# Kernel tuning notes

Measured on AMD Instinct MI355X. Metric: run time of the kernel, lower is better.

The kernel has to match this reference:

```python
import jax, jax.numpy as jnp
import numpy as np

N_NODES = 100000
N_EDGES = 3200000
NDIM_IN = 64
EDIM = 64
NDIM_OUT = 32
HID1, HID2 = 50, 25


def _linear_init(key, fan_in, fan_out):
    # torch nn.Linear default: U(-1/sqrt(fan_in), 1/sqrt(fan_in))
    kw, kb = jax.random.split(key)
    bound = 1.0 / np.sqrt(fan_in)
    W = jax.random.uniform(kw, (fan_in, fan_out), jnp.float32, -bound, bound)
    b = jax.random.uniform(kb, (fan_out,), jnp.float32, -bound, bound)
    return W, b


def setup_inputs() -> dict:
    key = jax.random.key(0)
    ks = jax.random.split(key, 10)
    nfeats = jax.random.normal(ks[0], (N_NODES, 1, NDIM_IN), jnp.float32)
    efeats = jax.random.normal(ks[1], (N_EDGES, 1, EDIM), jnp.float32)
    src = jax.random.randint(ks[2], (N_EDGES,), 0, N_NODES, jnp.int32)
    dst = jax.random.randint(ks[3], (N_EDGES,), 0, N_NODES, jnp.int32)
    Wm1, bm1 = _linear_init(ks[4], NDIM_IN + EDIM, HID1)
    Wa1, ba1 = _linear_init(ks[5], NDIM_IN + HID1, HID1)
    Wm2, bm2 = _linear_init(ks[6], HID1 + EDIM, HID2)
    Wa2, ba2 = _linear_init(ks[7], HID1 + HID2, HID2)
    Wm3, bm3 = _linear_init(ks[8], HID2 + EDIM, NDIM_OUT)
    Wa3, ba3 = _linear_init(ks[9], HID2 + NDIM_OUT, NDIM_OUT)
    return {
        "nfeats": nfeats, "efeats": efeats, "src": src, "dst": dst,
        "Wm1": Wm1, "bm1": bm1, "Wa1": Wa1, "ba1": ba1,
        "Wm2": Wm2, "bm2": bm2, "Wa2": Wa2, "ba2": ba2,
        "Wm3": Wm3, "bm3": bm3, "Wa3": Wa3, "ba3": ba3,
    }


def _gnn_layer(h, e, src, dst, Wm, bm, Wa, ba):
    # h: [N,1,Fin], e: [E,1,Fe]
    # per-edge message: relu(Linear(cat(h[src], e)))  -> [E,1,Fout]
    m = jax.nn.relu(jnp.concatenate([h[src], e], axis=-1) @ Wm + bm)
    # sum-aggregate messages per destination node -> [N,1,Fout]
    h_neigh = jax.ops.segment_sum(m, dst, num_segments=h.shape[0])
    # node apply: relu(Linear(cat(h, h_neigh)))
    return jax.nn.relu(jnp.concatenate([h, h_neigh], axis=-1) @ Wa + ba)


def reference(nfeats, efeats, src, dst,
              Wm1, bm1, Wa1, ba1,
              Wm2, bm2, Wa2, ba2,
              Wm3, bm3, Wa3, ba3):
    h = _gnn_layer(nfeats, efeats, src, dst, Wm1, bm1, Wa1, ba1)
    h = _gnn_layer(h, efeats, src, dst, Wm2, bm2, Wa2, ba2)  # dropout p=0.0
    h = _gnn_layer(h, efeats, src, dst, Wm3, bm3, Wa3, ba3)
    return h.sum(axis=1)  # [N, ndim_out]
```

## Files before the change

### kernel.cpp

```cpp
#include <hip/hip_runtime.h>

#define DEVINL __device__ __forceinline__

typedef __attribute__((ext_vector_type(8))) short bf16x8;
typedef __attribute__((ext_vector_type(4))) float f32x4;

DEVINL void fma4(float4& a, const float4 w, const float x) {
    a.x += w.x * x; a.y += w.y * x; a.z += w.z * x; a.w += w.w * x;
}

DEVINL unsigned short bf16of(float x) {
    unsigned a = __float_as_uint(x);
    a += 0x7FFFu + ((a >> 16) & 1u);
    return (unsigned short)(a >> 16);
}

DEVINL unsigned bfpair(float lo, float hi) {
    unsigned a = __float_as_uint(lo);
    a += 0x7FFFu + ((a >> 16) & 1u);
    unsigned b = __float_as_uint(hi);
    b += 0x7FFFu + ((b >> 16) & 1u);
    return (a >> 16) | (b & 0xFFFF0000u);
}

DEVINL float bflo(unsigned u) { return __uint_as_float(u << 16); }
DEVINL float bfhi(unsigned u) { return __uint_as_float(u & 0xFFFF0000u); }

DEVINL bf16x8 as_bf16x8(uint4 u) {
    union { uint4 u4; bf16x8 b; } cv; cv.u4 = u; return cv.b;
}

__global__ __launch_bounds__(256) void hist_kernel(const int* __restrict__ d,
                                                   int* __restrict__ counts, int n) {
    for (int i = blockIdx.x * 256 + threadIdx.x; i < n; i += gridDim.x * 256)
        atomicAdd(&counts[d[i]], 1);
}

__global__ __launch_bounds__(1024) void scan_block(const int* __restrict__ in,
                                                   int* __restrict__ out,
                                                   int* __restrict__ bsums, int n) {
    __shared__ int buf[2][1024];
    const int t = threadIdx.x;
    const int i = blockIdx.x * 1024 + t;
    const int v = (i < n) ? in[i] : 0;
    int cur = 0;
    buf[0][t] = v;
    __syncthreads();
    #pragma unroll
    for (int s = 1; s < 1024; s <<= 1) {
        int x = buf[cur][t];
        if (t >= s) x += buf[cur][t - s];
        buf[cur ^ 1][t] = x;
        cur ^= 1;
        __syncthreads();
    }
    if (i < n) out[i] = buf[cur][t] - v;
    if (t == 1023) bsums[blockIdx.x] = buf[cur][t];
}

__global__ void scan_small(int* __restrict__ bs, int nb) {
    if (blockIdx.x == 0 && threadIdx.x == 0) {
        int acc = 0;
        for (int i = 0; i < nb; i++) { int v = bs[i]; bs[i] = acc; acc += v; }
    }
}

__global__ __launch_bounds__(1024) void add_offsets(int* __restrict__ out,
                                                    const int* __restrict__ bs, int n) {
    int i = blockIdx.x * 1024 + threadIdx.x;
    if (i < n) out[i] += bs[blockIdx.x];
}

__global__ __launch_bounds__(256) void scatter_kernel(const int* __restrict__ d,
                                                      const int* __restrict__ src,
                                                      int* __restrict__ cursor,
                                                      int4* __restrict__ recs, int n) {
    for (int i = blockIdx.x * 256 + threadIdx.x; i < n; i += gridDim.x * 256) {
        int dd = d[i];
        int ss = src[i];
        int pos = atomicAdd(&cursor[dd], 1);
        recs[pos] = make_int4(i, dd, ss, 0);
    }
}

template<int FIN, int FOUT, int FOUTP>
__global__ __launch_bounds__(256) void pack_we(const float* __restrict__ W,
                                               float* __restrict__ Wp) {
    int idx = blockIdx.x * 256 + threadIdx.x;
    if (idx >= 64 * FOUTP) return;
    int k = idx / FOUTP, j = idx - k * FOUTP;
    Wp[idx] = (j < FOUT) ? W[(FIN + k) * FOUT + j] : 0.f;
}

template<int FIN, int FOUT, int NC>
__global__ __launch_bounds__(256) void pack_wbt(const float* __restrict__ W,
                                                unsigned short* __restrict__ WbT) {
    int idx = blockIdx.x * 256 + threadIdx.x;
    if (idx >= NC * 64) return;
    int c = idx / 64, k = idx - c * 64;
    WbT[idx] = (c < FOUT) ? bf16of(W[(FIN + k) * FOUT + c]) : (unsigned short)0;
}

template<int FIN, int FOUT, int FOUTP>
__global__ __launch_bounds__(256) void gemv_g(
    const float* __restrict__ x,
    const float* __restrict__ W,
    const float* __restrict__ b,
    float* __restrict__ g, int nNodes)
{
    constexpr int F4 = FOUTP / 4;
    __shared__ float4 Wl[FIN * F4];
    __shared__ float  bl[FOUTP];
    const int tid = threadIdx.x;
    for (int idx = tid; idx < FIN * FOUTP; idx += 256) {
        int k = idx / FOUTP, j = idx - k * FOUTP;
        reinterpret_cast<float*>(Wl)[idx] = (j < FOUT) ? W[k * FOUT + j] : 0.f;
    }
    for (int idx = tid; idx < FOUTP; idx += 256)
        bl[idx] = (idx < FOUT) ? b[idx] : 0.f;
    __syncthreads();
    const int n = blockIdx.x * 256 + tid;
    if (n >= nNodes) return;
    float4 acc[F4];
    #pragma unroll
    for (int j4 = 0; j4 < F4; j4++) acc[j4] = reinterpret_cast<float4*>(bl)[j4];
    const float* xr = x + (long long)n * FIN;
    #pragma unroll 1
    for (int k = 0; k < FIN; ++k) {
        float xk = xr[k];
        const float4* wrow = &Wl[k * F4];
        #pragma unroll
        for (int j4 = 0; j4 < F4; j4++) fma4(acc[j4], wrow[j4], xk);
    }
    float4* gr = reinterpret_cast<float4*>(g + (long long)n * FOUTP);
    #pragma unroll
    for (int j4 = 0; j4 < F4; j4++) gr[j4] = acc[j4];
}

__global__ __launch_bounds__(256) void edge_mfma_all(
    const float* __restrict__ g,
    const float* __restrict__ efeats,
    const int4* __restrict__ recs,
    const unsigned short* __restrict__ Wb1,
    const unsigned short* __restrict__ Wb2,
    const unsigned short* __restrict__ Wb3,
    unsigned* __restrict__ ep2,
    unsigned* __restrict__ ep3,
    float* __restrict__ agg)
{
    constexpr int FOUT = 50, FOUTP = 52, NT = 4;
    constexpr int MS = NT * 16 + 1;

    __shared__ float msg[4][32 * MS];
    __shared__ int eidL[512], sIdxL[512], dseg[512];

    const int tid = threadIdx.x;
    const long long pb = (long long)blockIdx.x * 512;
    {
        int4 r0 = recs[pb + tid];
        int4 r1 = recs[pb + 256 + tid];
        eidL[tid] = r0.x;  dseg[tid] = r0.y;  sIdxL[tid] = r0.z;
        eidL[tid + 256] = r1.x; dseg[tid + 256] = r1.y; sIdxL[tid + 256] = r1.z;
    }
    __syncthreads();

    const int lane = tid & 63;
    const int wv   = tid >> 6;
    const int lg   = lane >> 4;
    const int lc   = lane & 15;

    bf16x8 bfr1[2][4], bfr2[2][2], bfr3[2][2];
    #pragma unroll
    for (int kt = 0; kt < 2; kt++) {
        #pragma unroll
        for (int nt = 0; nt < 4; nt++)
            bfr1[kt][nt] = *reinterpret_cast<const bf16x8*>(Wb1 + (nt * 16 + lc) * 64 + kt * 32 + lg * 8);
        #pragma unroll
        for (int nt = 0; nt < 2; nt++) {
            bfr2[kt][nt] = *reinterpret_cast<const bf16x8*>(Wb2 + (nt * 16 + lc) * 64 + kt * 32 + lg * 8);
            bfr3[kt][nt] = *reinterpret_cast<const bf16x8*>(Wb3 + (nt * 16 + lc) * 64 + kt * 32 + lg * 8);
        }
    }

    float* msgW = msg[wv];

    #pragma unroll 1
    for (int ch = 0; ch < 4; ++ch) {
        const int rb0 = wv * 128 + ch * 32;
        #pragma unroll 1
        for (int mt = 0; mt < 2; ++mt) {
            const int rowbase = rb0 + mt * 16;
            const long long tix = (pb >> 4) + wv * 8 + ch * 2 + mt;
            const int eid = eidL[rowbase + lc];
            const float4* erow = reinterpret_cast<const float4*>(efeats + (long long)eid * 64);
            float4 f0 = erow[lg * 2];
            float4 f1 = erow[lg * 2 + 1];
            float4 f2 = erow[8 + lg * 2];
            float4 f3 = erow[8 + lg * 2 + 1];
            uint4 u0, u1;
            u0.x = bfpair(f0.x, f0.y); u0.y = bfpair(f0.z, f0.w);
            u0.z = bfpair(f1.x, f1.y); u0.w = bfpair(f1.z, f1.w);
            u1.x = bfpair(f2.x, f2.y); u1.y = bfpair(f2.z, f2.w);
            u1.z = bfpair(f3.x, f3.y); u1.w = bfpair(f3.z, f3.w);
            bf16x8 a0 = as_bf16x8(u0);
            bf16x8 a1 = as_bf16x8(u1);

            int sr[4];
            #pragma unroll
            for (int r = 0; r < 4; r++) sr[r] = sIdxL[rowbase + lg * 4 + r];

            #pragma unroll
            for (int nt = 0; nt < 4; nt++) {
                f32x4 acc = {0.f, 0.f, 0.f, 0.f};
                acc = __builtin_amdgcn_mfma_f32_16x16x32_bf16(a0, bfr1[0][nt], acc, 0, 0, 0);
                acc = __builtin_amdgcn_mfma_f32_16x16x32_bf16(a1, bfr1[1][nt], acc, 0, 0, 0);
                const int col = nt * 16 + lc;
                #pragma unroll
                for (int r = 0; r < 4; r++) {
                    float gv = (col < FOUT) ? g[(long long)sr[r] * FOUTP + col] : 0.f;
                    msgW[(mt * 16 + lg * 4 + r) * MS + col] = fmaxf(acc[r] + gv, 0.f);
                }
            }
            {
                uint4 st;
                #pragma unroll
                for (int nt = 0; nt < 2; nt++) {
                    f32x4 acc = {0.f, 0.f, 0.f, 0.f};
                    acc = __builtin_amdgcn_mfma_f32_16x16x32_bf16(a0, bfr2[0][nt], acc, 0, 0, 0);
                    acc = __builtin_amdgcn_mfma_f32_16x16x32_bf16(a1, bfr2[1][nt], acc, 0, 0, 0);
                    unsigned w0 = bfpair(acc[0], acc[1]);
                    unsigned w1 = bfpair(acc[2], acc[3]);
                    if (nt == 0) { st.x = w0; st.y = w1; } else { st.z = w0; st.w = w1; }
                }
                reinterpret_cast<uint4*>(ep2)[tix * 64 + lane] = st;
            }
            {
                uint4 st;
                #pragma unroll
                for (int nt = 0; nt < 2; nt++) {
                    f32x4 acc = {0.f, 0.f, 0.f, 0.f};
                    acc = __builtin_amdgcn_mfma_f32_16x16x32_bf16(a0, bfr3[0][nt], acc, 0, 0, 0);
                    acc = __builtin_amdgcn_mfma_f32_16x16x32_bf16(a1, bfr3[1][nt], acc, 0, 0, 0);
                    unsigned w0 = bfpair(acc[0], acc[1]);
                    unsigned w1 = bfpair(acc[2], acc[3]);
                    if (nt == 0) { st.x = w0; st.y = w1; } else { st.z = w0; st.w = w1; }
                }
                reinterpret_cast<uint4*>(ep3)[tix * 64 + lane] = st;
            }
        }
        const int base = rb0;
        for (int r0 = 0; r0 < 32; ++r0) {
            int dr = dseg[base + r0];
            if (r0 > 0 && dseg[base + r0 - 1] == dr) continue;
            float s = 0.f;
            int rr = r0;
            while (true) {
                s += msgW[rr * MS + lane];
                ++rr;
                if (rr >= 32 || dseg[base + rr] != dr) break;
            }
            if (lane < FOUT) atomicAdd(agg + (long long)dr * FOUT + lane, s);
        }
    }
}

template<int FOUT, int FOUTP>
__global__ __launch_bounds__(256) void edge_ep(
    const float* __restrict__ g,
    const unsigned* __restrict__ ep,
    const int4* __restrict__ recs,
    float* __restrict__ agg)
{
    constexpr int NT = 2;
    constexpr int MS = NT * 16 + 1;

    __shared__ float msg[4][32 * MS];
    __shared__ int sIdxL[512], dseg[512];

    const int tid = threadIdx.x;
    const long long pb = (long long)blockIdx.x * 512;
    {
        int4 r0 = recs[pb + tid];
        int4 r1 = recs[pb + 256 + tid];
        dseg[tid] = r0.y;  sIdxL[tid] = r0.z;
        dseg[tid + 256] = r1.y; sIdxL[tid + 256] = r1.z;
    }
    __syncthreads();

    const int lane = tid & 63;
    const int wv   = tid >> 6;
    const int lg   = lane >> 4;
    const int lc   = lane & 15;

    float* msgW = msg[wv];

    #pragma unroll 1
    for (int ch = 0; ch < 4; ++ch) {
        const int rb0 = wv * 128 + ch * 32;
        #pragma unroll
        for (int mt = 0; mt < 2; ++mt) {
            const int rowbase = rb0 + mt * 16;
            const long long tix = (pb >> 4) + wv * 8 + ch * 2 + mt;
            uint4 v = reinterpret_cast<const uint4*>(ep)[tix * 64 + lane];

            int sr[4];
            #pragma unroll
            for (int r = 0; r < 4; r++) sr[r] = sIdxL[rowbase + lg * 4 + r];

            #pragma unroll
            for (int nt = 0; nt < 2; nt++) {
                float e0 = bflo(nt == 0 ? v.x : v.z);
                float e1 = bfhi(nt == 0 ? v.x : v.z);
                float e2 = bflo(nt == 0 ? v.y : v.w);
                float e3 = bfhi(nt == 0 ? v.y : v.w);
                const int col = nt * 16 + lc;
                float ev[4] = {e0, e1, e2, e3};
                #pragma unroll
                for (int r = 0; r < 4; r++) {
                    float gv = (col < FOUT) ? g[(long long)sr[r] * FOUTP + col] : 0.f;
                    msgW[(mt * 16 + lg * 4 + r) * MS + col] = fmaxf(ev[r] + gv, 0.f);
                }
            }
        }
        const int base = rb0;
        for (int r0 = 0; r0 < 32; ++r0) {
            int dr = dseg[base + r0];
            if (r0 > 0 && dseg[base + r0 - 1] == dr) continue;
            float s = 0.f;
            int rr = r0;
            while (true) {
                s += msgW[rr * MS + lane];
                ++rr;
                if (rr >= 32 || dseg[base + rr] != dr) break;
            }
            if (lane < FOUT) atomicAdd(agg + (long long)dr * FOUT + lane, s);
        }
    }
}

template<int FOUT, int FOUTP, int MS>
__global__ __launch_bounds__(256) void edge_fb(
    const float* __restrict__ g,
    const float* __restrict__ efeats,
    const int4* __restrict__ recs,
    const float* __restrict__ Wp,
    float* __restrict__ agg)
{
    constexpr int F4 = FOUTP / 4;
    constexpr int ST = 17;
    static_assert(128 * MS + 64 <= 512 * ST, "msg buf exceeds sbuf");

    __shared__ float sbuf[512 * ST];
    __shared__ int   dseg[512];

    const int tid = threadIdx.x;
    const long long pb = (long long)blockIdx.x * 512;
    int4 r0 = recs[pb + tid];
    int4 r1 = recs[pb + 256 + tid];
    dseg[tid] = r0.y;
    dseg[tid + 256] = r1.y;

    const float4* gr0 = reinterpret_cast<const float4*>(g + (long long)r0.z * FOUTP);
    const float4* gr1 = reinterpret_cast<const float4*>(g + (long long)r1.z * FOUTP);
    const float*  er0 = efeats + (long long)r0.x * 64;
    const float*  er1 = efeats + (long long)r1.x * 64;
    const float4* Wp4 = reinterpret_cast<const float4*>(Wp);

    float4 acc0[F4], acc1[F4];
    #pragma unroll
    for (int j4 = 0; j4 < F4; j4++) acc0[j4] = gr0[j4];
    #pragma unroll
    for (int j4 = 0; j4 < F4; j4++) acc1[j4] = gr1[j4];

    const int t0 = tid * ST;
    const int t1 = (tid + 256) * ST;

    for (int c = 0; c < 4; ++c) {
        const int off = c * 16;
        #pragma unroll
        for (int f = 0; f < 4; ++f) {
            float4 v0 = *reinterpret_cast<const float4*>(er0 + off + 4 * f);
            float4 v1 = *reinterpret_cast<const float4*>(er1 + off + 4 * f);
            float* d0 = &sbuf[t0 + 4 * f];
            float* d1 = &sbuf[t1 + 4 * f];
            d0[0] = v0.x; d0[1] = v0.y; d0[2] = v0.z; d0[3] = v0.w;
            d1[0] = v1.x; d1[1] = v1.y; d1[2] = v1.z; d1[3] = v1.w;
        }
        #pragma unroll 1
        for (int k = 0; k < 16; ++k) {
            const float x0 = sbuf[t0 + k];
            const float x1 = sbuf[t1 + k];
            const float4* wrow = &Wp4[(off + k) * F4];
            #pragma unroll
            for (int j4 = 0; j4 < F4; j4++) {
                float4 w = wrow[j4];
                fma4(acc0[j4], w, x0);
                fma4(acc1[j4], w, x1);
            }
        }
    }

    const int lane = tid & 63;
    const int wv   = tid >> 6;

    #pragma unroll 1
    for (int bb = 0; bb < 4; ++bb) {
        __syncthreads();
        if ((tid >> 7) == (bb & 1)) {
            const int r = tid & 127;
            float* mrow = &sbuf[r * MS];
            const float4* accp = (bb < 2) ? acc0 : acc1;
            #pragma unroll
            for (int j4 = 0; j4 < F4; j4++) {
                float4 a = accp[j4];
                if (4 * j4 + 0 < FOUT) mrow[4 * j4 + 0] = fmaxf(a.x, 0.f);
                if (4 * j4 + 1 < FOUT) mrow[4 * j4 + 1] = fmaxf(a.y, 0.f);
                if (4 * j4 + 2 < FOUT) mrow[4 * j4 + 2] = fmaxf(a.z, 0.f);
                if (4 * j4 + 3 < FOUT) mrow[4 * j4 + 3] = fmaxf(a.w, 0.f);
            }
        }
        __syncthreads();

        const int rbase = bb * 128;
        for (int r0i = wv * 32; r0i < wv * 32 + 32; ++r0i) {
            int dr = dseg[rbase + r0i];
            if (r0i > 0 && dseg[rbase + r0i - 1] == dr) continue;
            float s = 0.f;
            int rr = r0i;
            while (true) {
                s += sbuf[rr * MS + lane];
                ++rr;
                if (rr >= 128 || dseg[rbase + rr] != dr) break;
            }
            if (lane < FOUT) atomicAdd(agg + (long long)dr * FOUT + lane, s);
        }
    }
}

template<int FH, int FHP, int FAGG, int FOUT, int FOUTP, int GOUT, int GOUTP>
__global__ __launch_bounds__(256) void node_kernel(
    const float* __restrict__ h,
    const float* __restrict__ agg,
    const float* __restrict__ Wa,
    const float* __restrict__ ba,
    const float* __restrict__ Wmn,
    const float* __restrict__ bmn,
    float* __restrict__ out,
    float* __restrict__ gout,
    int nNodes)
{
    constexpr int K  = FH + FAGG;
    constexpr int F4 = FOUTP / 4;
    constexpr int G4 = (GOUT > 0) ? GOUTP / 4 : 1;

    __shared__ float4 Wl[K * F4];
    __shared__ float4 Wg[(GOUT > 0) ? FOUTP * G4 : 1];
    __shared__ float  bl[FOUTP];
    __shared__ float  bg[(GOUT > 0) ? GOUTP : 4];

    const int tid = threadIdx.x;
    for (int idx = tid; idx < K * FOUTP; idx += 256) {
        int k = idx / FOUTP, j = idx - k * FOUTP;
        reinterpret_cast<float*>(Wl)[idx] = (j < FOUT) ? Wa[k * FOUT + j] : 0.f;
    }
    for (int idx = tid; idx < FOUTP; idx += 256)
        bl[idx] = (idx < FOUT) ? ba[idx] : 0.f;
    if constexpr (GOUT > 0) {
        for (int idx = tid; idx < FOUTP * GOUTP; idx += 256) {
            int k = idx / GOUTP, j = idx - k * GOUTP;
            reinterpret_cast<float*>(Wg)[idx] =
                (k < FOUT && j < GOUT) ? Wmn[k * GOUT + j] : 0.f;
        }
        for (int idx = tid; idx < GOUTP; idx += 256)
            bg[idx] = (idx < GOUT) ? bmn[idx] : 0.f;
    }
    __syncthreads();

    const int n = blockIdx.x * 256 + tid;
    if (n >= nNodes) return;

    float4 acc[F4];
    #pragma unroll
    for (int j4 = 0; j4 < F4; j4++) acc[j4] = reinterpret_cast<float4*>(bl)[j4];

    const float* hrow = h + (long long)n * FHP;
    #pragma unroll 1
    for (int k = 0; k < FH; k++) {
        float xk = hrow[k];
        const float4* wrow = &Wl[k * F4];
        #pragma unroll
        for (int j4 = 0; j4 < F4; j4++) fma4(acc[j4], wrow[j4], xk);
    }
    const float* arow = agg + (long long)n * FAGG;
    #pragma unroll 1
    for (int k = 0; k < FAGG; k++) {
        float xk = arow[k];
        const float4* wrow = &Wl[(FH + k) * F4];
        #pragma unroll
        for (int j4 = 0; j4 < F4; j4++) fma4(acc[j4], wrow[j4], xk);
    }

    #pragma unroll
    for (int j4 = 0; j4 < F4; j4++) {
        acc[j4].x = fmaxf(acc[j4].x, 0.f);
        acc[j4].y = fmaxf(acc[j4].y, 0.f);
        acc[j4].z = fmaxf(acc[j4].z, 0.f);
        acc[j4].w = fmaxf(acc[j4].w, 0.f);
    }
    float4* orow = reinterpret_cast<float4*>(out + (long long)n * FOUTP);
    #pragma unroll
    for (int j4 = 0; j4 < F4; j4++) orow[j4] = acc[j4];

    if constexpr (GOUT > 0) {
        float4 gacc[G4];
        #pragma unroll
        for (int j4 = 0; j4 < G4; j4++) gacc[j4] = reinterpret_cast<float4*>(bg)[j4];
        #pragma unroll 1
        for (int k4 = 0; k4 < F4; ++k4) {
            float4 xv = acc[k4];
            #pragma unroll
            for (int c = 0; c < 4; ++c) {
                float xc = (c == 0) ? xv.x : (c == 1) ? xv.y : (c == 2) ? xv.z : xv.w;
                const float4* wrow = &Wg[(k4 * 4 + c) * G4];
                #pragma unroll
                for (int j4 = 0; j4 < G4; j4++) fma4(gacc[j4], wrow[j4], xc);
            }
        }
        float4* grow = reinterpret_cast<float4*>(gout + (long long)n * GOUTP);
        #pragma unroll
        for (int j4 = 0; j4 < G4; j4++) grow[j4] = gacc[j4];
    }
}

extern "C" void kernel_launch(void* const* d_in, const int* in_sizes, int n_in,
                              void* d_out, int out_size, void* d_ws, size_t ws_size,
                              hipStream_t stream)
{
    const float* nfeats = (const float*)d_in[0];
    const float* efeats = (const float*)d_in[1];
    const int*   src    = (const int*)d_in[2];
    const int*   dst    = (const int*)d_in[3];
    const float* Wm1 = (const float*)d_in[4],  *bm1 = (const float*)d_in[5];
    const float* Wa1 = (const float*)d_in[6],  *ba1 = (const float*)d_in[7];
    const float* Wm2 = (const float*)d_in[8],  *bm2 = (const float*)d_in[9];
    const float* Wa2 = (const float*)d_in[10], *ba2 = (const float*)d_in[11];
    const float* Wm3 = (const float*)d_in[12], *bm3 = (const float*)d_in[13];
    const float* Wa3 = (const float*)d_in[14], *ba3 = (const float*)d_in[15];
    float* out = (float*)d_out;

    constexpr int N = 100000;
    constexpr int E = 3200000;
    constexpr int SCAN_BLOCKS = (N + 1023) / 1024;

    float* ws   = (float*)d_ws;
    float* h1   = ws;
    float* h2   = h1 + (size_t)N * 52;
    float* agg  = h2 + (size_t)N * 28;
    float* g    = agg + (size_t)N * 52;
    int* counts = (int*)(g + (size_t)N * 52);
    int* cursor = counts + N;
    int* bsums  = cursor + N;
    int4* recs  = (int4*)(bsums + 128);
    float* Wp1  = (float*)(recs + E);
    float* Wp2  = Wp1 + 64 * 52;
    float* Wp3  = Wp2 + 64 * 28;
    unsigned short* Wb1 = (unsigned short*)(Wp3 + 64 * 32);
    unsigned short* Wb2 = Wb1 + 64 * 64;
    unsigned short* Wb3 = Wb2 + 32 * 64;
    char* endp = (char*)(Wb3 + 32 * 64);

    size_t usedB  = (size_t)(endp - (char*)d_ws);
    size_t epOffB = (usedB + 127) & ~(size_t)127;
    size_t neededB = epOffB + (size_t)E * 128;
    const bool useBf = (ws_size >= neededB);
    unsigned* ep2 = (unsigned*)((char*)d_ws + epOffB);
    unsigned* ep3 = ep2 + (size_t)E * 16;

    pack_we<64, 50, 52><<<(64 * 52 + 255) / 256, 256, 0, stream>>>(Wm1, Wp1);
    pack_we<50, 25, 28><<<(64 * 28 + 255) / 256, 256, 0, stream>>>(Wm2, Wp2);
    pack_we<25, 32, 32><<<(64 * 32 + 255) / 256, 256, 0, stream>>>(Wm3, Wp3);
    pack_wbt<64, 50, 64><<<(64 * 64 + 255) / 256, 256, 0, stream>>>(Wm1, Wb1);
    pack_wbt<50, 25, 32><<<(32 * 64 + 255) / 256, 256, 0, stream>>>(Wm2, Wb2);
    pack_wbt<25, 32, 32><<<(32 * 64 + 255) / 256, 256, 0, stream>>>(Wm3, Wb3);

    hipMemsetAsync(counts, 0, (size_t)N * sizeof(int), stream);
    hist_kernel<<<2048, 256, 0, stream>>>(dst, counts, E);
    scan_block<<<SCAN_BLOCKS, 1024, 0, stream>>>(counts, cursor, bsums, N);
    scan_small<<<1, 64, 0, stream>>>(bsums, SCAN_BLOCKS);
    add_offsets<<<SCAN_BLOCKS, 1024, 0, stream>>>(cursor, bsums, N);
    scatter_kernel<<<2048, 256, 0, stream>>>(dst, src, cursor, recs, E);

    const int EB = E / 512;
    const int NB = (N + 255) / 256;

    gemv_g<64, 50, 52><<<NB, 256, 0, stream>>>(nfeats, Wm1, bm1, g, N);

    hipMemsetAsync(agg, 0, (size_t)N * 52 * sizeof(float), stream);
    if (useBf)
        edge_mfma_all<<<EB, 256, 0, stream>>>(g, efeats, recs, Wb1, Wb2, Wb3, ep2, ep3, agg);
    else
        edge_fb<50, 52, 51><<<EB, 256, 0, stream>>>(g, efeats, recs, Wp1, agg);
    node_kernel<64, 64, 50, 50, 52, 25, 28><<<NB, 256, 0, stream>>>(
        nfeats, agg, Wa1, ba1, Wm2, bm2, h1, g, N);

    hipMemsetAsync(agg, 0, (size_t)N * 52 * sizeof(float), stream);
    if (useBf)
        edge_ep<25, 28><<<EB, 256, 0, stream>>>(g, ep2, recs, agg);
    else
        edge_fb<25, 28, 25><<<EB, 256, 0, stream>>>(g, efeats, recs, Wp2, agg);
    node_kernel<50, 52, 25, 25, 28, 32, 32><<<NB, 256, 0, stream>>>(
        h1, agg, Wa2, ba2, Wm3, bm3, h2, g, N);

    hipMemsetAsync(agg, 0, (size_t)N * 52 * sizeof(float), stream);
    if (useBf)
        edge_ep<32, 32><<<EB, 256, 0, stream>>>(g, ep3, recs, agg);
    else
        edge_fb<32, 32, 33><<<EB, 256, 0, stream>>>(g, efeats, recs, Wp3, agg);
    node_kernel<25, 28, 32, 32, 32, 0, 0><<<NB, 256, 0, stream>>>(
        h2, agg, Wa3, ba3, nullptr, nullptr, out, nullptr, N);
}
```

Baseline: 1.551 ms.

## Software-pipeline edge feature and gathered node loads across chunks in edge kernels

```diff
diff --git a/kernel.cpp b/kernel.cpp
--- a/kernel.cpp
+++ b/kernel.cpp
@@ -184,30 +184,49 @@
 
     float* msgW = msg[wv];
 
+    float4 f[2][4];
+    {
+        const int rb0 = wv * 128;
+        #pragma unroll
+        for (int mt = 0; mt < 2; mt++) {
+            const int eid = eidL[rb0 + mt * 16 + lc];
+            const float4* erow = reinterpret_cast<const float4*>(efeats + (long long)eid * 64);
+            f[mt][0] = erow[lg * 2];     f[mt][1] = erow[lg * 2 + 1];
+            f[mt][2] = erow[8 + lg * 2]; f[mt][3] = erow[8 + lg * 2 + 1];
+        }
+    }
+
     #pragma unroll 1
     for (int ch = 0; ch < 4; ++ch) {
         const int rb0 = wv * 128 + ch * 32;
-        #pragma unroll 1
-        for (int mt = 0; mt < 2; ++mt) {
-            const int rowbase = rb0 + mt * 16;
-            const long long tix = (pb >> 4) + wv * 8 + ch * 2 + mt;
-            const int eid = eidL[rowbase + lc];
-            const float4* erow = reinterpret_cast<const float4*>(efeats + (long long)eid * 64);
-            float4 f0 = erow[lg * 2];
-            float4 f1 = erow[lg * 2 + 1];
-            float4 f2 = erow[8 + lg * 2];
-            float4 f3 = erow[8 + lg * 2 + 1];
+
+        int srr[2][4];
+        #pragma unroll
+        for (int mt = 0; mt < 2; mt++)
+            #pragma unroll
+            for (int r = 0; r < 4; r++)
+                srr[mt][r] = sIdxL[rb0 + mt * 16 + lg * 4 + r];
+        float gv[2][NT][4];
+        #pragma unroll
+        for (int mt = 0; mt < 2; mt++)
+            #pragma unroll
+            for (int nt = 0; nt < NT; nt++) {
+                const int col = nt * 16 + lc;
+                #pragma unroll
+                for (int r = 0; r < 4; r++)
+                    gv[mt][nt][r] = (col < FOUT) ? g[(long long)srr[mt][r] * FOUTP + col] : 0.f;
+            }
+
+        #pragma unroll
+        for (int mt = 0; mt < 2; mt++) {
             uint4 u0, u1;
-            u0.x = bfpair(f0.x, f0.y); u0.y = bfpair(f0.z, f0.w);
-            u0.z = bfpair(f1.x, f1.y); u0.w = bfpair(f1.z, f1.w);
-            u1.x = bfpair(f2.x, f2.y); u1.y = bfpair(f2.z, f2.w);
-            u1.z = bfpair(f3.x, f3.y); u1.w = bfpair(f3.z, f3.w);
+            u0.x = bfpair(f[mt][0].x, f[mt][0].y); u0.y = bfpair(f[mt][0].z, f[mt][0].w);
+            u0.z = bfpair(f[mt][1].x, f[mt][1].y); u0.w = bfpair(f[mt][1].z, f[mt][1].w);
+            u1.x = bfpair(f[mt][2].x, f[mt][2].y); u1.y = bfpair(f[mt][2].z, f[mt][2].w);
+            u1.z = bfpair(f[mt][3].x, f[mt][3].y); u1.w = bfpair(f[mt][3].z, f[mt][3].w);
             bf16x8 a0 = as_bf16x8(u0);
             bf16x8 a1 = as_bf16x8(u1);
-
-            int sr[4];
-            #pragma unroll
-            for (int r = 0; r < 4; r++) sr[r] = sIdxL[rowbase + lg * 4 + r];
+            const long long tix = (pb >> 4) + wv * 8 + ch * 2 + mt;
 
             #pragma unroll
             for (int nt = 0; nt < 4; nt++) {
@@ -216,10 +235,8 @@
                 acc = __builtin_amdgcn_mfma_f32_16x16x32_bf16(a1, bfr1[1][nt], acc, 0, 0, 0);
                 const int col = nt * 16 + lc;
                 #pragma unroll
-                for (int r = 0; r < 4; r++) {
-                    float gv = (col < FOUT) ? g[(long long)sr[r] * FOUTP + col] : 0.f;
-                    msgW[(mt * 16 + lg * 4 + r) * MS + col] = fmaxf(acc[r] + gv, 0.f);
-                }
+                for (int r = 0; r < 4; r++)
+                    msgW[(mt * 16 + lg * 4 + r) * MS + col] = fmaxf(acc[r] + gv[mt][nt][r], 0.f);
             }
             {
                 uint4 st;
@@ -248,6 +265,19 @@
                 reinterpret_cast<uint4*>(ep3)[tix * 64 + lane] = st;
             }
         }
+
+        float4 fn[2][4];
+        if (ch < 3) {
+            const int rbn = wv * 128 + (ch + 1) * 32;
+            #pragma unroll
+            for (int mt = 0; mt < 2; mt++) {
+                const int eid = eidL[rbn + mt * 16 + lc];
+                const float4* erow = reinterpret_cast<const float4*>(efeats + (long long)eid * 64);
+                fn[mt][0] = erow[lg * 2];     fn[mt][1] = erow[lg * 2 + 1];
+                fn[mt][2] = erow[8 + lg * 2]; fn[mt][3] = erow[8 + lg * 2 + 1];
+            }
+        }
+
         const int base = rb0;
         for (int r0 = 0; r0 < 32; ++r0) {
             int dr = dseg[base + r0];
@@ -261,6 +291,13 @@
             }
             if (lane < FOUT) atomicAdd(agg + (long long)dr * FOUT + lane, s);
         }
+
+        if (ch < 3) {
+            #pragma unroll
+            for (int mt = 0; mt < 2; mt++)
+                #pragma unroll
+                for (int q = 0; q < 4; q++) f[mt][q] = fn[mt][q];
+        }
     }
 }
 
@@ -294,34 +331,64 @@
 
     float* msgW = msg[wv];
 
+    uint4 v[2];
+    float gv[2][2][4];
+    {
+        const int rb0 = wv * 128;
+        #pragma unroll
+        for (int mt = 0; mt < 2; mt++) {
+            const long long tix = (pb >> 4) + wv * 8 + mt;
+            v[mt] = reinterpret_cast<const uint4*>(ep)[tix * 64 + lane];
+            #pragma unroll
+            for (int nt = 0; nt < 2; nt++) {
+                const int col = nt * 16 + lc;
+                #pragma unroll
+                for (int r = 0; r < 4; r++) {
+                    int sr = sIdxL[rb0 + mt * 16 + lg * 4 + r];
+                    gv[mt][nt][r] = (col < FOUT) ? g[(long long)sr * FOUTP + col] : 0.f;
+                }
+            }
+        }
+    }
+
     #pragma unroll 1
     for (int ch = 0; ch < 4; ++ch) {
         const int rb0 = wv * 128 + ch * 32;
-        #pragma unroll
-        for (int mt = 0; mt < 2; ++mt) {
-            const int rowbase = rb0 + mt * 16;
-            const long long tix = (pb >> 4) + wv * 8 + ch * 2 + mt;
-            uint4 v = reinterpret_cast<const uint4*>(ep)[tix * 64 + lane];
-
-            int sr[4];
-            #pragma unroll
-            for (int r = 0; r < 4; r++) sr[r] = sIdxL[rowbase + lg * 4 + r];
-
+
+        #pragma unroll
+        for (int mt = 0; mt < 2; mt++) {
             #pragma unroll
             for (int nt = 0; nt < 2; nt++) {
-                float e0 = bflo(nt == 0 ? v.x : v.z);
-                float e1 = bfhi(nt == 0 ? v.x : v.z);
-                float e2 = bflo(nt == 0 ? v.y : v.w);
-                float e3 = bfhi(nt == 0 ? v.y : v.w);
+                unsigned w0 = (nt == 0) ? v[mt].x : v[mt].z;
+                unsigned w1 = (nt == 0) ? v[mt].y : v[mt].w;
+                float ev[4] = {bflo(w0), bfhi(w0), bflo(w1), bfhi(w1)};
                 const int col = nt * 16 + lc;
-                float ev[4] = {e0, e1, e2, e3};
-                #pragma unroll
-                for (int r = 0; r < 4; r++) {
-                    float gv = (col < FOUT) ? g[(long long)sr[r] * FOUTP + col] : 0.f;
-                    msgW[(mt * 16 + lg * 4 + r) * MS + col] = fmaxf(ev[r] + gv, 0.f);
+                #pragma unroll
+                for (int r = 0; r < 4; r++)
+                    msgW[(mt * 16 + lg * 4 + r) * MS + col] = fmaxf(ev[r] + gv[mt][nt][r], 0.f);
+            }
+        }
+
+        uint4 vn[2];
+        float gvn[2][2][4];
+        if (ch < 3) {
+            const int rbn = wv * 128 + (ch + 1) * 32;
+            #pragma unroll
+            for (int mt = 0; mt < 2; mt++) {
+                const long long tix = (pb >> 4) + wv * 8 + (ch + 1) * 2 + mt;
+                vn[mt] = reinterpret_cast<const uint4*>(ep)[tix * 64 + lane];
+                #pragma unroll
+                for (int nt = 0; nt < 2; nt++) {
+                    const int col = nt * 16 + lc;
+                    #pragma unroll
+                    for (int r = 0; r < 4; r++) {
+                        int sr = sIdxL[rbn + mt * 16 + lg * 4 + r];
+                        gvn[mt][nt][r] = (col < FOUT) ? g[(long long)sr * FOUTP + col] : 0.f;
+                    }
                 }
             }
         }
+
         const int base = rb0;
         for (int r0 = 0; r0 < 32; ++r0) {
             int dr = dseg[base + r0];
@@ -329,11 +396,22 @@
             float s = 0.f;
             int rr = r0;
             while (true) {
-                s += msgW[rr * MS + lane];
+                if (lane < NT * 16) s += msgW[rr * MS + lane];
                 ++rr;
                 if (rr >= 32 || dseg[base + rr] != dr) break;
             }
             if (lane < FOUT) atomicAdd(agg + (long long)dr * FOUT + lane, s);
+        }
+
+        if (ch < 3) {
+            #pragma unroll
+            for (int mt = 0; mt < 2; mt++) {
+                v[mt] = vn[mt];
+                #pragma unroll
+                for (int nt = 0; nt < 2; nt++)
+                    #pragma unroll
+                    for (int r = 0; r < 4; r++) gv[mt][nt][r] = gvn[mt][nt][r];
+            }
         }
     }
 }
```

After: 1.398 ms. -9.9%, faster.
